# Performance work log

Measured on AMD Instinct MI355X. Metric: run time of the kernel, lower is better.

The kernel has to match this reference:

```python
import jax, jax.numpy as jnp
import numpy as np

N = 40000
E = 640000
F_IN = 128
HID = 64
HEADS = 4
NUM_CLASSES = 40
NEG_SLOPE = 0.2  # GATConv default leaky_relu slope


def setup_inputs() -> dict:
    key = jax.random.key(0)
    ks = jax.random.split(key, 10)
    glorot = lambda k, shape: (jax.random.uniform(k, shape, jnp.float32) * 2.0 - 1.0) * jnp.sqrt(6.0 / (shape[0] + shape[-1]))
    x = jax.random.normal(ks[0], (N, F_IN), jnp.float32)
    edge_index = jax.random.randint(ks[1], (2, E), 0, N, jnp.int64)
    # layer 1: in=128 -> heads=4, out=64, concat
    W1 = glorot(ks[2], (F_IN, HEADS * HID))
    att_src1 = glorot(ks[3], (HEADS, HID))
    att_dst1 = glorot(ks[4], (HEADS, HID))
    b1 = jnp.zeros((HEADS * HID,), jnp.float32)
    # layer 2: in=256 -> heads=1, out=num_classes
    W2 = glorot(ks[5], (HEADS * HID, 1 * NUM_CLASSES))
    att_src2 = glorot(ks[6], (1, NUM_CLASSES))
    att_dst2 = glorot(ks[7], (1, NUM_CLASSES))
    b2 = jnp.zeros((NUM_CLASSES,), jnp.float32)
    return {"x": x, "edge_index": edge_index, "W1": W1, "att_src1": att_src1,
            "att_dst1": att_dst1, "b1": b1, "W2": W2, "att_src2": att_src2,
            "att_dst2": att_dst2, "b2": b2}


def gat_conv(x, src, dst, W, att_src, att_dst, bias, heads, out_ch, n_nodes):
    """PyG GATConv (add_self_loops applied by caller, dropout=eval/no-op)."""
    h = (x @ W).reshape(n_nodes, heads, out_ch)            # [N, H, C]
    a_src = jnp.einsum('nhc,hc->nh', h, att_src)            # [N, H]
    a_dst = jnp.einsum('nhc,hc->nh', h, att_dst)            # [N, H]
    e = jax.nn.leaky_relu(a_src[src] + a_dst[dst], NEG_SLOPE)  # [E', H]
    # segment softmax over incoming edges of each destination node
    m = jax.ops.segment_max(e, dst, num_segments=n_nodes)   # [N, H]
    p = jnp.exp(e - m[dst])
    z = jax.ops.segment_sum(p, dst, num_segments=n_nodes)   # [N, H]
    alpha = p / z[dst]                                      # [E', H]
    msg = h[src] * alpha[:, :, None]                        # [E', H, C]
    out = jax.ops.segment_sum(msg, dst, num_segments=n_nodes)  # [N, H, C]
    return out.reshape(n_nodes, heads * out_ch) + bias


def reference(x, edge_index, W1, att_src1, att_dst1, b1, W2, att_src2, att_dst2, b2):
    loop = jnp.arange(N, dtype=edge_index.dtype)
    src = jnp.concatenate([edge_index[0], loop])
    dst = jnp.concatenate([edge_index[1], loop])
    h = gat_conv(x, src, dst, W1, att_src1, att_dst1, b1, HEADS, HID, N)
    h = jax.nn.relu(h)  # dropout is identity in eval mode
    h = gat_conv(h, src, dst, W2, att_src2, att_dst2, b2, 1, NUM_CLASSES, N)
    return jax.nn.log_softmax(h, axis=1)
```

## Files before the change

kernel.cpp:

```cpp
#include <hip/hip_runtime.h>
#include <math.h>

#define NEG_SLOPE 0.2f

typedef unsigned short ushort_t;
typedef __attribute__((ext_vector_type(8))) short short8v;
typedef __attribute__((ext_vector_type(4))) float f32x4;

__device__ inline ushort_t f2bf(float f) {
    unsigned b = __float_as_uint(f);
    unsigned r = (b + 0x7fffu + ((b >> 16) & 1u)) >> 16;
    return (ushort_t)r;
}
__device__ inline float bf2f(ushort_t u) { return __uint_as_float(((unsigned)u) << 16); }
__device__ inline float bflo(unsigned w) { return __uint_as_float(w << 16); }
__device__ inline float bfhi(unsigned w) { return __uint_as_float(w & 0xffff0000u); }

__global__ void hist_kernel(const int* __restrict__ ei, int E, int EP, int* __restrict__ deg)
{
    int e = blockIdx.x * 256 + threadIdx.x;
    if (e >= EP) return;
    int d = (e < E) ? ei[E + e] : (e - E);
    atomicAdd(&deg[d], 1);
}

__global__ void block_sum_kernel(const int* __restrict__ deg, int* __restrict__ bsum, int N)
{
    int i = blockIdx.x * 256 + threadIdx.x;
    int v = (i < N) ? deg[i] : 0;
#pragma unroll
    for (int off = 32; off > 0; off >>= 1) v += __shfl_xor(v, off, 64);
    __shared__ int wsum[4];
    if ((threadIdx.x & 63) == 0) wsum[threadIdx.x >> 6] = v;
    __syncthreads();
    if (threadIdx.x == 0) bsum[blockIdx.x] = wsum[0] + wsum[1] + wsum[2] + wsum[3];
}

__global__ void scan_bsum_kernel(int* __restrict__ bsum, int* __restrict__ totalp, int nb)
{
    __shared__ int sh[256];
    int tid = threadIdx.x;
    int v = (tid < nb) ? bsum[tid] : 0;
    sh[tid] = v;
    __syncthreads();
    for (int off = 1; off < 256; off <<= 1) {
        int t = (tid >= off) ? sh[tid - off] : 0;
        __syncthreads();
        sh[tid] += t;
        __syncthreads();
    }
    if (tid < nb) bsum[tid] = sh[tid] - v;
    if (tid == 255) *totalp = sh[255];
}

__global__ void block_scan_kernel(const int* __restrict__ deg, const int* __restrict__ bsum,
                                  int* __restrict__ rowptr, int N)
{
    __shared__ int sh[256];
    int i = blockIdx.x * 256 + threadIdx.x;
    int tid = threadIdx.x;
    int v = (i < N) ? deg[i] : 0;
    sh[tid] = v;
    __syncthreads();
    for (int off = 1; off < 256; off <<= 1) {
        int t = (tid >= off) ? sh[tid - off] : 0;
        __syncthreads();
        sh[tid] += t;
        __syncthreads();
    }
    if (i < N) rowptr[i] = bsum[blockIdx.x] + sh[tid] - v;
}

__global__ void scatter_kernel(const int* __restrict__ ei, int E, int EP,
                               const int* __restrict__ rowptr, int* __restrict__ deg,
                               int* __restrict__ colsrc)
{
    int e = blockIdx.x * 256 + threadIdx.x;
    if (e >= EP) return;
    int s, d;
    if (e < E) { s = ei[e]; d = ei[E + e]; } else { s = e - E; d = e - E; }
    int old = atomicSub(&deg[d], 1);
    colsrc[rowptr[d] + old - 1] = s;
}

__global__ void prepack_kernel(const float* __restrict__ W1, const float* __restrict__ W2,
                               ushort_t* __restrict__ w1p, ushort_t* __restrict__ w2p)
{
    int i = blockIdx.x * 256 + threadIdx.x;
    if (i < 32768) {
        int j = i & 7, lane = (i >> 3) & 63, t = i >> 9;
        int kt = t >> 4, nt = t & 15;
        int k = kt * 32 + (lane >> 4) * 8 + j;
        int n = nt * 16 + (lane & 15);
        w1p[i] = f2bf(W1[k * 256 + n]);
    } else {
        int ii = i - 32768;
        if (ii < 12288) {
            int j = ii & 7, lane = (ii >> 3) & 63, t = ii >> 9;
            int kt = t / 3, nt = t - kt * 3;
            int k = kt * 32 + (lane >> 4) * 8 + j;
            int n = nt * 16 + (lane & 15);
            w2p[ii] = (n < 40) ? f2bf(W2[k * 40 + n]) : (ushort_t)0;
        }
    }
}

__global__ __launch_bounds__(256) void gemm1_mfma(
    const float* __restrict__ x, const ushort_t* __restrict__ w1p,
    const float* __restrict__ att_src, const float* __restrict__ att_dst,
    ushort_t* __restrict__ h1b, float* __restrict__ asrc, float* __restrict__ adst, int N)
{
    __shared__ ushort_t xs[64][136];
    const int n0 = blockIdx.x * 64;
    const int tid = threadIdx.x;
    const int lane = tid & 63;
    const int w = tid >> 6;
    const int l16 = lane & 15;
    const int g = lane >> 4;

#pragma unroll
    for (int it = 0; it < 8; it++) {
        int idx = tid + it * 256;
        int row = idx >> 5, c4 = (idx & 31) * 4;
        float4 v = *(const float4*)(x + (size_t)(n0 + row) * 128 + c4);
        ushort4 u = {f2bf(v.x), f2bf(v.y), f2bf(v.z), f2bf(v.w)};
        *(ushort4*)&xs[row][c4] = u;
    }
    __syncthreads();

    short8v afr[4];
#pragma unroll
    for (int kt = 0; kt < 4; kt++)
        afr[kt] = *(const short8v*)&xs[w * 16 + l16][kt * 32 + g * 8];

    f32x4 acc[16];
#pragma unroll
    for (int nt = 0; nt < 16; nt++) acc[nt] = (f32x4){0.f, 0.f, 0.f, 0.f};

    const short8v* wp = (const short8v*)w1p;
#pragma unroll
    for (int nt = 0; nt < 16; nt++) {
        short8v b0 = wp[(0 * 16 + nt) * 64 + lane];
        short8v b1 = wp[(1 * 16 + nt) * 64 + lane];
        short8v b2 = wp[(2 * 16 + nt) * 64 + lane];
        short8v b3 = wp[(3 * 16 + nt) * 64 + lane];
        acc[nt] = __builtin_amdgcn_mfma_f32_16x16x32_bf16(afr[0], b0, acc[nt], 0, 0, 0);
        acc[nt] = __builtin_amdgcn_mfma_f32_16x16x32_bf16(afr[1], b1, acc[nt], 0, 0, 0);
        acc[nt] = __builtin_amdgcn_mfma_f32_16x16x32_bf16(afr[2], b2, acc[nt], 0, 0, 0);
        acc[nt] = __builtin_amdgcn_mfma_f32_16x16x32_bf16(afr[3], b3, acc[nt], 0, 0, 0);
    }

    float ps[4][4], pd[4][4];
#pragma unroll
    for (int r = 0; r < 4; r++)
#pragma unroll
        for (int h = 0; h < 4; h++) { ps[r][h] = 0.f; pd[r][h] = 0.f; }

#pragma unroll
    for (int nt = 0; nt < 16; nt++) {
        const int col = nt * 16 + l16;
        const float as_c = att_src[col];
        const float ad_c = att_dst[col];
        const int h = nt >> 2;
#pragma unroll
        for (int r = 0; r < 4; r++) {
            float v = acc[nt][r];
            h1b[(size_t)(n0 + w * 16 + g * 4 + r) * 256 + col] = f2bf(v);
            ps[r][h] += v * as_c;
            pd[r][h] += v * ad_c;
        }
    }
#pragma unroll
    for (int r = 0; r < 4; r++)
#pragma unroll
        for (int h = 0; h < 4; h++)
#pragma unroll
            for (int off = 8; off > 0; off >>= 1) {
                ps[r][h] += __shfl_xor(ps[r][h], off, 64);
                pd[r][h] += __shfl_xor(pd[r][h], off, 64);
            }

    const int sel = l16 >> 2;
#pragma unroll
    for (int hh = 0; hh < 4; hh++) {
        if (hh == (l16 & 3)) {
            if (sel == 0) {
#pragma unroll
                for (int r = 0; r < 4; r++)
                    asrc[(size_t)(n0 + w * 16 + g * 4 + r) * 4 + hh] = ps[r][hh];
            } else if (sel == 1) {
#pragma unroll
                for (int r = 0; r < 4; r++)
                    adst[(size_t)(n0 + w * 16 + g * 4 + r) * 4 + hh] = pd[r][hh];
            }
        }
    }
}

__global__ __launch_bounds__(256) void node_agg1(
    const int* __restrict__ rowptr, const int* __restrict__ colsrc,
    const float* __restrict__ asrc, const float* __restrict__ adst,
    const ushort_t* __restrict__ h1b, const float* __restrict__ b1,
    float* __restrict__ a1, int N)
{
    int n = (blockIdx.x * 256 + threadIdx.x) >> 6;
    int lane = threadIdx.x & 63;
    if (n >= N) return;
    const int r0 = rowptr[n], r1 = rowptr[n + 1];
    const int half = lane >> 5;
    const int l5 = lane & 31;
    const int head = l5 >> 3;
    const int coff = head * 64 + (l5 & 7) * 8;
    const float adhh = adst[(size_t)n * 4 + head];

    float acc[8] = {0.f, 0.f, 0.f, 0.f, 0.f, 0.f, 0.f, 0.f};
    float ssum = 0.f;
    int j = r0;
    for (; j + 8 <= r1; j += 8) {
        int jA = j + half, jB = j + 2 + half, jC = j + 4 + half, jD = j + 6 + half;
        int sA = colsrc[jA], sB = colsrc[jB], sC = colsrc[jC], sD = colsrc[jD];
        float aA = asrc[(size_t)sA * 4 + head];
        float aB = asrc[(size_t)sB * 4 + head];
        float aC = asrc[(size_t)sC * 4 + head];
        float aD = asrc[(size_t)sD * 4 + head];
        uint4 qA = *(const uint4*)&h1b[(size_t)sA * 256 + coff];
        uint4 qB = *(const uint4*)&h1b[(size_t)sB * 256 + coff];
        uint4 qC = *(const uint4*)&h1b[(size_t)sC * 256 + coff];
        uint4 qD = *(const uint4*)&h1b[(size_t)sD * 256 + coff];
        float vA = aA + adhh; vA = vA > 0.f ? vA : NEG_SLOPE * vA;
        float vB = aB + adhh; vB = vB > 0.f ? vB : NEG_SLOPE * vB;
        float vC = aC + adhh; vC = vC > 0.f ? vC : NEG_SLOPE * vC;
        float vD = aD + adhh; vD = vD > 0.f ? vD : NEG_SLOPE * vD;
        float pA = __expf(vA), pB = __expf(vB), pC = __expf(vC), pD = __expf(vD);
        ssum += (pA + pB) + (pC + pD);
        acc[0] += pA * bflo(qA.x) + pB * bflo(qB.x) + pC * bflo(qC.x) + pD * bflo(qD.x);
        acc[1] += pA * bfhi(qA.x) + pB * bfhi(qB.x) + pC * bfhi(qC.x) + pD * bfhi(qD.x);
        acc[2] += pA * bflo(qA.y) + pB * bflo(qB.y) + pC * bflo(qC.y) + pD * bflo(qD.y);
        acc[3] += pA * bfhi(qA.y) + pB * bfhi(qB.y) + pC * bfhi(qC.y) + pD * bfhi(qD.y);
        acc[4] += pA * bflo(qA.z) + pB * bflo(qB.z) + pC * bflo(qC.z) + pD * bflo(qD.z);
        acc[5] += pA * bfhi(qA.z) + pB * bfhi(qB.z) + pC * bfhi(qC.z) + pD * bfhi(qD.z);
        acc[6] += pA * bflo(qA.w) + pB * bflo(qB.w) + pC * bflo(qC.w) + pD * bflo(qD.w);
        acc[7] += pA * bfhi(qA.w) + pB * bfhi(qB.w) + pC * bfhi(qC.w) + pD * bfhi(qD.w);
    }
    for (; j < r1; j += 2) {
        int jj = j + half;
        bool valid = jj < r1;
        int s = colsrc[valid ? jj : r0];
        float a = asrc[(size_t)s * 4 + head];
        uint4 q = *(const uint4*)&h1b[(size_t)s * 256 + coff];
        float v = a + adhh; v = v > 0.f ? v : NEG_SLOPE * v;
        float p = valid ? __expf(v) : 0.f;
        ssum += p;
        acc[0] += p * bflo(q.x);
        acc[1] += p * bfhi(q.x);
        acc[2] += p * bflo(q.y);
        acc[3] += p * bfhi(q.y);
        acc[4] += p * bflo(q.z);
        acc[5] += p * bfhi(q.z);
        acc[6] += p * bflo(q.w);
        acc[7] += p * bfhi(q.w);
    }

#pragma unroll
    for (int k = 0; k < 8; k++) acc[k] += __shfl_xor(acc[k], 32, 64);
    ssum += __shfl_xor(ssum, 32, 64);
    const float rz = 1.f / ssum;

    float s0 = half ? acc[4] : acc[0];
    float s1 = half ? acc[5] : acc[1];
    float s2 = half ? acc[6] : acc[2];
    float s3 = half ? acc[7] : acc[3];
    const int wc = coff + half * 4;
    const float4 bv = *(const float4*)&b1[wc];
    float o0 = s0 * rz + bv.x;
    float o1 = s1 * rz + bv.y;
    float o2 = s2 * rz + bv.z;
    float o3 = s3 * rz + bv.w;
    float4 outv = make_float4(o0 > 0.f ? o0 : 0.f, o1 > 0.f ? o1 : 0.f,
                              o2 > 0.f ? o2 : 0.f, o3 > 0.f ? o3 : 0.f);
    *(float4*)&a1[(size_t)n * 256 + wc] = outv;
}

__global__ __launch_bounds__(256) void gemm2_mfma(
    const float* __restrict__ A, const ushort_t* __restrict__ w2p,
    const float* __restrict__ as2, const float* __restrict__ ad2,
    ushort_t* __restrict__ h2b, float* __restrict__ asrc, float* __restrict__ adst, int N)
{
    __shared__ ushort_t xs[64][264];
    const int n0 = blockIdx.x * 64;
    const int tid = threadIdx.x;
    const int lane = tid & 63;
    const int w = tid >> 6;
    const int l16 = lane & 15;
    const int g = lane >> 4;

#pragma unroll
    for (int it = 0; it < 16; it++) {
        int idx = tid + it * 256;
        int row = idx >> 6, c4 = (idx & 63) * 4;
        float4 v = *(const float4*)(A + (size_t)(n0 + row) * 256 + c4);
        ushort4 u = {f2bf(v.x), f2bf(v.y), f2bf(v.z), f2bf(v.w)};
        *(ushort4*)&xs[row][c4] = u;
    }
    __syncthreads();

    short8v afr[8];
#pragma unroll
    for (int kt = 0; kt < 8; kt++)
        afr[kt] = *(const short8v*)&xs[w * 16 + l16][kt * 32 + g * 8];

    f32x4 acc[3];
#pragma unroll
    for (int nt = 0; nt < 3; nt++) acc[nt] = (f32x4){0.f, 0.f, 0.f, 0.f};

    const short8v* wp = (const short8v*)w2p;
#pragma unroll
    for (int nt = 0; nt < 3; nt++) {
#pragma unroll
        for (int kt = 0; kt < 8; kt++) {
            short8v b = wp[(kt * 3 + nt) * 64 + lane];
            acc[nt] = __builtin_amdgcn_mfma_f32_16x16x32_bf16(afr[kt], b, acc[nt], 0, 0, 0);
        }
    }

    float ps[4] = {0.f, 0.f, 0.f, 0.f}, pd[4] = {0.f, 0.f, 0.f, 0.f};
#pragma unroll
    for (int nt = 0; nt < 3; nt++) {
        const int col = nt * 16 + l16;
        const bool ok = col < 40;
        const float as_c = ok ? as2[col] : 0.f;
        const float ad_c = ok ? ad2[col] : 0.f;
#pragma unroll
        for (int r = 0; r < 4; r++) {
            float v = acc[nt][r];
            if (ok) h2b[(size_t)(n0 + w * 16 + g * 4 + r) * 40 + col] = f2bf(v);
            ps[r] += v * as_c;
            pd[r] += v * ad_c;
        }
    }
#pragma unroll
    for (int r = 0; r < 4; r++)
#pragma unroll
        for (int off = 8; off > 0; off >>= 1) {
            ps[r] += __shfl_xor(ps[r], off, 64);
            pd[r] += __shfl_xor(pd[r], off, 64);
        }
    if (l16 == 0) {
#pragma unroll
        for (int r = 0; r < 4; r++) asrc[n0 + w * 16 + g * 4 + r] = ps[r];
    } else if (l16 == 1) {
#pragma unroll
        for (int r = 0; r < 4; r++) adst[n0 + w * 16 + g * 4 + r] = pd[r];
    }
}

__global__ __launch_bounds__(256) void node_agg2(
    const int* __restrict__ rowptr, const int* __restrict__ colsrc,
    const float* __restrict__ asrc, const float* __restrict__ adst,
    const ushort_t* __restrict__ h2b, const float* __restrict__ b2,
    float* __restrict__ out, int N)
{
    int n = (blockIdx.x * 256 + threadIdx.x) >> 6;
    int lane = threadIdx.x & 63;
    if (n >= N) return;
    const int r0 = rowptr[n], r1 = rowptr[n + 1];
    const int half = lane >> 5;
    const int l5 = lane & 31;
    const bool act = l5 < 20;
    const int cc = act ? 2 * l5 : 0;
    const float ad = adst[n];

    float acc0 = 0.f, acc1 = 0.f, ssum = 0.f;
    int j = r0;
    for (; j + 8 <= r1; j += 8) {
        int jA = j + half, jB = j + 2 + half, jC = j + 4 + half, jD = j + 6 + half;
        int sA = colsrc[jA], sB = colsrc[jB], sC = colsrc[jC], sD = colsrc[jD];
        float eA = asrc[sA] + ad, eB = asrc[sB] + ad, eC = asrc[sC] + ad, eD = asrc[sD] + ad;
        unsigned qA = *(const unsigned*)&h2b[(size_t)sA * 40 + cc];
        unsigned qB = *(const unsigned*)&h2b[(size_t)sB * 40 + cc];
        unsigned qC = *(const unsigned*)&h2b[(size_t)sC * 40 + cc];
        unsigned qD = *(const unsigned*)&h2b[(size_t)sD * 40 + cc];
        eA = eA > 0.f ? eA : NEG_SLOPE * eA;
        eB = eB > 0.f ? eB : NEG_SLOPE * eB;
        eC = eC > 0.f ? eC : NEG_SLOPE * eC;
        eD = eD > 0.f ? eD : NEG_SLOPE * eD;
        float pA = __expf(eA), pB = __expf(eB), pC = __expf(eC), pD = __expf(eD);
        ssum += (pA + pB) + (pC + pD);
        acc0 += pA * bflo(qA) + pB * bflo(qB) + pC * bflo(qC) + pD * bflo(qD);
        acc1 += pA * bfhi(qA) + pB * bfhi(qB) + pC * bfhi(qC) + pD * bfhi(qD);
    }
    for (; j < r1; j += 2) {
        int jj = j + half;
        bool valid = jj < r1;
        int s = colsrc[valid ? jj : r0];
        float e = asrc[s] + ad;
        unsigned q = *(const unsigned*)&h2b[(size_t)s * 40 + cc];
        e = e > 0.f ? e : NEG_SLOPE * e;
        float p = valid ? __expf(e) : 0.f;
        ssum += p;
        acc0 += p * bflo(q);
        acc1 += p * bfhi(q);
    }

    acc0 += __shfl_xor(acc0, 32, 64);
    acc1 += __shfl_xor(acc1, 32, 64);
    ssum += __shfl_xor(ssum, 32, 64);
    const float rz = 1.f / ssum;

    float v0 = act ? acc0 * rz + b2[cc]     : -1.0e30f;
    float v1 = act ? acc1 * rz + b2[cc + 1] : -1.0e30f;
    float mx = fmaxf(v0, v1);
#pragma unroll
    for (int off = 16; off > 0; off >>= 1) mx = fmaxf(mx, __shfl_xor(mx, off, 64));
    float pe = act ? __expf(v0 - mx) + __expf(v1 - mx) : 0.f;
#pragma unroll
    for (int off = 16; off > 0; off >>= 1) pe += __shfl_xor(pe, off, 64);
    float lse = mx + logf(pe);
    if (act && half == 0) {
        float2 o = make_float2(v0 - lse, v1 - lse);
        *(float2*)&out[(size_t)n * 40 + cc] = o;
    }
}

extern "C" void kernel_launch(void* const* d_in, const int* in_sizes, int n_in,
                              void* d_out, int out_size, void* d_ws, size_t ws_size,
                              hipStream_t stream)
{
    const float* x   = (const float*)d_in[0];
    const int*   ei  = (const int*)d_in[1];
    const float* W1  = (const float*)d_in[2];
    const float* as1 = (const float*)d_in[3];
    const float* ad1 = (const float*)d_in[4];
    const float* b1  = (const float*)d_in[5];
    const float* W2  = (const float*)d_in[6];
    const float* as2 = (const float*)d_in[7];
    const float* ad2 = (const float*)d_in[8];
    const float* b2  = (const float*)d_in[9];
    float* out = (float*)d_out;

    const int N  = in_sizes[0] / 128;
    const int E  = in_sizes[1] / 2;
    const int EP = E + N;
    const int NB = (N + 255) / 256;

    char* ws = (char*)d_ws;
    ushort_t* h1b  = (ushort_t*)ws;
    float* a1      = (float*)(ws + (size_t)N * 256 * 2);
    float* asrc    = a1 + (size_t)N * 256;
    float* adst    = asrc + (size_t)N * 4;
    int*   rowptr  = (int*)(adst + (size_t)N * 4);
    int*   colsrc  = rowptr + (N + 1);
    int*   deg     = colsrc + EP;
    ushort_t* h2b  = (ushort_t*)(deg + N);
    int*   bsum    = (int*)(h2b + (size_t)N * 40 + 16);
    ushort_t* w1p  = (ushort_t*)(bsum + NB);
    ushort_t* w2p  = w1p + 32768;

    hipMemsetAsync(deg, 0, (size_t)N * sizeof(int), stream);
    int egrid = (EP + 255) / 256;
    prepack_kernel<<<(32768 + 12288 + 255) / 256, 256, 0, stream>>>(W1, W2, w1p, w2p);
    hist_kernel<<<egrid, 256, 0, stream>>>(ei, E, EP, deg);
    block_sum_kernel<<<NB, 256, 0, stream>>>(deg, bsum, N);
    scan_bsum_kernel<<<1, 256, 0, stream>>>(bsum, rowptr + N, NB);
    block_scan_kernel<<<NB, 256, 0, stream>>>(deg, bsum, rowptr, N);
    scatter_kernel<<<egrid, 256, 0, stream>>>(ei, E, EP, rowptr, deg, colsrc);

    gemm1_mfma<<<N / 64, 256, 0, stream>>>(x, w1p, as1, ad1, h1b, asrc, adst, N);
    node_agg1<<<(N * 64 + 255) / 256, 256, 0, stream>>>(rowptr, colsrc, asrc, adst, h1b, b1, a1, N);

    gemm2_mfma<<<N / 64, 256, 0, stream>>>(a1, w2p, as2, ad2, h2b, asrc, adst, N);
    node_agg2<<<(N * 64 + 255) / 256, 256, 0, stream>>>(rowptr, colsrc, asrc, adst, h2b, b2, out, N);
}
```

Baseline: 189.3 us.

## Store layer-1 output as bf16 and fuse prepack and scan launches

The layer-1 aggregation now writes its activations as bf16 instead of fp32, and the second GEMM loads them directly without converting. This halves the intermediate write and read traffic (about 40 MB down to 20 MB). Weight prepacking is folded into the histogram kernel, and the single-block scan of block sums is merged into the per-block scan, with each block redundantly scanning all block sums. Together these remove two kernel launches. The bf16 rounding happens at the same point as before, since gemm2 already converted to bf16, so numerics should be unchanged.

Measured after the change: 182.3 us, median of 2. 1.04x faster.

```diff
diff --git a/kernel.cpp b/kernel.cpp
--- a/kernel.cpp
+++ b/kernel.cpp
@@ -16,12 +16,30 @@
 __device__ inline float bflo(unsigned w) { return __uint_as_float(w << 16); }
 __device__ inline float bfhi(unsigned w) { return __uint_as_float(w & 0xffff0000u); }
 
-__global__ void hist_kernel(const int* __restrict__ ei, int E, int EP, int* __restrict__ deg)
+__global__ void hist_prepack_kernel(const int* __restrict__ ei, int E, int EP,
+                                    int* __restrict__ deg,
+                                    const float* __restrict__ W1, const float* __restrict__ W2,
+                                    ushort_t* __restrict__ w1p, ushort_t* __restrict__ w2p)
 {
     int e = blockIdx.x * 256 + threadIdx.x;
-    if (e >= EP) return;
-    int d = (e < E) ? ei[E + e] : (e - E);
-    atomicAdd(&deg[d], 1);
+    if (e < EP) {
+        int d = (e < E) ? ei[E + e] : (e - E);
+        atomicAdd(&deg[d], 1);
+    }
+    if (e < 32768) {
+        int j = e & 7, lane = (e >> 3) & 63, t = e >> 9;
+        int kt = t >> 4, nt = t & 15;
+        int k = kt * 32 + (lane >> 4) * 8 + j;
+        int n = nt * 16 + (lane & 15);
+        w1p[e] = f2bf(W1[k * 256 + n]);
+    } else if (e < 32768 + 12288) {
+        int ii = e - 32768;
+        int j = ii & 7, lane = (ii >> 3) & 63, t = ii >> 9;
+        int kt = t / 3, nt = t - kt * 3;
+        int k = kt * 32 + (lane >> 4) * 8 + j;
+        int n = nt * 16 + (lane & 15);
+        w2p[ii] = (n < 40) ? f2bf(W2[k * 40 + n]) : (ushort_t)0;
+    }
 }
 
 __global__ void block_sum_kernel(const int* __restrict__ deg, int* __restrict__ bsum, int N)
@@ -36,39 +54,29 @@
     if (threadIdx.x == 0) bsum[blockIdx.x] = wsum[0] + wsum[1] + wsum[2] + wsum[3];
 }
 
-__global__ void scan_bsum_kernel(int* __restrict__ bsum, int* __restrict__ totalp, int nb)
-{
+__global__ void block_scan_kernel(const int* __restrict__ deg, const int* __restrict__ bsum,
+                                  int* __restrict__ rowptr, int N, int nb)
+{
+    __shared__ int sb[256];
     __shared__ int sh[256];
-    int tid = threadIdx.x;
-    int v = (tid < nb) ? bsum[tid] : 0;
-    sh[tid] = v;
-    __syncthreads();
-    for (int off = 1; off < 256; off <<= 1) {
-        int t = (tid >= off) ? sh[tid - off] : 0;
-        __syncthreads();
-        sh[tid] += t;
-        __syncthreads();
-    }
-    if (tid < nb) bsum[tid] = sh[tid] - v;
-    if (tid == 255) *totalp = sh[255];
-}
-
-__global__ void block_scan_kernel(const int* __restrict__ deg, const int* __restrict__ bsum,
-                                  int* __restrict__ rowptr, int N)
-{
-    __shared__ int sh[256];
-    int i = blockIdx.x * 256 + threadIdx.x;
-    int tid = threadIdx.x;
+    const int tid = threadIdx.x;
+    int bv = (tid < nb) ? bsum[tid] : 0;
+    sb[tid] = bv;
+    int i = blockIdx.x * 256 + tid;
     int v = (i < N) ? deg[i] : 0;
     sh[tid] = v;
     __syncthreads();
     for (int off = 1; off < 256; off <<= 1) {
-        int t = (tid >= off) ? sh[tid - off] : 0;
+        int tb = (tid >= off) ? sb[tid - off] : 0;
+        int tv = (tid >= off) ? sh[tid - off] : 0;
         __syncthreads();
-        sh[tid] += t;
+        sb[tid] += tb;
+        sh[tid] += tv;
         __syncthreads();
     }
-    if (i < N) rowptr[i] = bsum[blockIdx.x] + sh[tid] - v;
+    int blkoff = (blockIdx.x == 0) ? 0 : sb[blockIdx.x - 1];
+    if (i < N) rowptr[i] = blkoff + sh[tid] - v;
+    if (blockIdx.x == 0 && tid == 0) rowptr[N] = sb[nb - 1];
 }
 
 __global__ void scatter_kernel(const int* __restrict__ ei, int E, int EP,
@@ -81,28 +89,6 @@
     if (e < E) { s = ei[e]; d = ei[E + e]; } else { s = e - E; d = e - E; }
     int old = atomicSub(&deg[d], 1);
     colsrc[rowptr[d] + old - 1] = s;
-}
-
-__global__ void prepack_kernel(const float* __restrict__ W1, const float* __restrict__ W2,
-                               ushort_t* __restrict__ w1p, ushort_t* __restrict__ w2p)
-{
-    int i = blockIdx.x * 256 + threadIdx.x;
-    if (i < 32768) {
-        int j = i & 7, lane = (i >> 3) & 63, t = i >> 9;
-        int kt = t >> 4, nt = t & 15;
-        int k = kt * 32 + (lane >> 4) * 8 + j;
-        int n = nt * 16 + (lane & 15);
-        w1p[i] = f2bf(W1[k * 256 + n]);
-    } else {
-        int ii = i - 32768;
-        if (ii < 12288) {
-            int j = ii & 7, lane = (ii >> 3) & 63, t = ii >> 9;
-            int kt = t / 3, nt = t - kt * 3;
-            int k = kt * 32 + (lane >> 4) * 8 + j;
-            int n = nt * 16 + (lane & 15);
-            w2p[ii] = (n < 40) ? f2bf(W2[k * 40 + n]) : (ushort_t)0;
-        }
-    }
 }
 
 __global__ __launch_bounds__(256) void gemm1_mfma(
@@ -201,7 +187,7 @@
     const int* __restrict__ rowptr, const int* __restrict__ colsrc,
     const float* __restrict__ asrc, const float* __restrict__ adst,
     const ushort_t* __restrict__ h1b, const float* __restrict__ b1,
-    float* __restrict__ a1, int N)
+    ushort_t* __restrict__ a1b, int N)
 {
     int n = (blockIdx.x * 256 + threadIdx.x) >> 6;
     int lane = threadIdx.x & 63;
@@ -276,13 +262,13 @@
     float o1 = s1 * rz + bv.y;
     float o2 = s2 * rz + bv.z;
     float o3 = s3 * rz + bv.w;
-    float4 outv = make_float4(o0 > 0.f ? o0 : 0.f, o1 > 0.f ? o1 : 0.f,
-                              o2 > 0.f ? o2 : 0.f, o3 > 0.f ? o3 : 0.f);
-    *(float4*)&a1[(size_t)n * 256 + wc] = outv;
+    ushort4 outv = {f2bf(o0 > 0.f ? o0 : 0.f), f2bf(o1 > 0.f ? o1 : 0.f),
+                    f2bf(o2 > 0.f ? o2 : 0.f), f2bf(o3 > 0.f ? o3 : 0.f)};
+    *(ushort4*)&a1b[(size_t)n * 256 + wc] = outv;
 }
 
 __global__ __launch_bounds__(256) void gemm2_mfma(
-    const float* __restrict__ A, const ushort_t* __restrict__ w2p,
+    const ushort_t* __restrict__ A, const ushort_t* __restrict__ w2p,
     const float* __restrict__ as2, const float* __restrict__ ad2,
     ushort_t* __restrict__ h2b, float* __restrict__ asrc, float* __restrict__ adst, int N)
 {
@@ -295,12 +281,11 @@
     const int g = lane >> 4;
 
 #pragma unroll
-    for (int it = 0; it < 16; it++) {
+    for (int it = 0; it < 8; it++) {
         int idx = tid + it * 256;
-        int row = idx >> 6, c4 = (idx & 63) * 4;
-        float4 v = *(const float4*)(A + (size_t)(n0 + row) * 256 + c4);
-        ushort4 u = {f2bf(v.x), f2bf(v.y), f2bf(v.z), f2bf(v.w)};
-        *(ushort4*)&xs[row][c4] = u;
+        int row = idx >> 5, c8 = (idx & 31) * 8;
+        uint4 v = *(const uint4*)(A + (size_t)(n0 + row) * 256 + c8);
+        *(uint4*)&xs[row][c8] = v;
     }
     __syncthreads();
 
@@ -445,8 +430,8 @@
 
     char* ws = (char*)d_ws;
     ushort_t* h1b  = (ushort_t*)ws;
-    float* a1      = (float*)(ws + (size_t)N * 256 * 2);
-    float* asrc    = a1 + (size_t)N * 256;
+    ushort_t* a1b  = h1b + (size_t)N * 256;
+    float* asrc    = (float*)(a1b + (size_t)N * 256);
     float* adst    = asrc + (size_t)N * 4;
     int*   rowptr  = (int*)(adst + (size_t)N * 4);
     int*   colsrc  = rowptr + (N + 1);
@@ -458,16 +443,14 @@
 
     hipMemsetAsync(deg, 0, (size_t)N * sizeof(int), stream);
     int egrid = (EP + 255) / 256;
-    prepack_kernel<<<(32768 + 12288 + 255) / 256, 256, 0, stream>>>(W1, W2, w1p, w2p);
-    hist_kernel<<<egrid, 256, 0, stream>>>(ei, E, EP, deg);
+    hist_prepack_kernel<<<egrid, 256, 0, stream>>>(ei, E, EP, deg, W1, W2, w1p, w2p);
     block_sum_kernel<<<NB, 256, 0, stream>>>(deg, bsum, N);
-    scan_bsum_kernel<<<1, 256, 0, stream>>>(bsum, rowptr + N, NB);
-    block_scan_kernel<<<NB, 256, 0, stream>>>(deg, bsum, rowptr, N);
+    block_scan_kernel<<<NB, 256, 0, stream>>>(deg, bsum, rowptr, N, NB);
     scatter_kernel<<<egrid, 256, 0, stream>>>(ei, E, EP, rowptr, deg, colsrc);
 
     gemm1_mfma<<<N / 64, 256, 0, stream>>>(x, w1p, as1, ad1, h1b, asrc, adst, N);
-    node_agg1<<<(N * 64 + 255) / 256, 256, 0, stream>>>(rowptr, colsrc, asrc, adst, h1b, b1, a1, N);
-
-    gemm2_mfma<<<N / 64, 256, 0, stream>>>(a1, w2p, as2, ad2, h2b, asrc, adst, N);
+    node_agg1<<<(N * 64 + 255) / 256, 256, 0, stream>>>(rowptr, colsrc, asrc, adst, h1b, b1, a1b, N);
+
+    gemm2_mfma<<<N / 64, 256, 0, stream>>>(a1b, w2p, as2, ad2, h2b, asrc, adst, N);
     node_agg2<<<(N * 64 + 255) / 256, 256, 0, stream>>>(rowptr, colsrc, asrc, adst, h2b, b2, out, N);
 }
```
